# Kernel optimization log

Measured on AMD Instinct MI355X. Metric: run time of the kernel, lower is better.

Reference implementation:

```python
import jax, jax.numpy as jnp
import numpy as np

N, IN, HID, HEADS, OUT, E = 50000, 128, 64, 4, 128, 800000
NEG_SLOPE = 0.2


def _gat_conv(x, src, dst, W, a_src, a_dst, b, heads, ch, concat):
    # x: [N, F_in]; W: [F_in, heads*ch]; a_src/a_dst: [heads, ch]; b: [heads*ch] or [ch]
    n = x.shape[0]
    h = (x @ W).reshape(n, heads, ch)                       # [N,H,C]
    al_s = jnp.einsum('nhc,hc->nh', h, a_src)               # [N,H]
    al_d = jnp.einsum('nhc,hc->nh', h, a_dst)               # [N,H]
    e = jax.nn.leaky_relu(al_s[src] + al_d[dst], NEG_SLOPE)  # [E,H]
    # segment softmax over destination nodes (every node has a self-loop)
    m = jax.ops.segment_max(e, dst, num_segments=n)
    ex = jnp.exp(e - m[dst])
    denom = jax.ops.segment_sum(ex, dst, num_segments=n)
    alpha = ex / denom[dst]                                  # [E,H]
    msg = h[src] * alpha[:, :, None]                         # [E,H,C]
    out = jax.ops.segment_sum(msg, dst, num_segments=n)      # [N,H,C]
    out = out.reshape(n, heads * ch) if concat else out.mean(axis=1)
    return out + b


def setup_inputs() -> dict:
    key = jax.random.key(0)
    ks = jax.random.split(key, 10)
    s = 0.1
    return {
        'node_features': jax.random.normal(ks[0], (N, IN), jnp.float32),
        'edge_index': jax.random.randint(ks[1], (2, E), 0, N, jnp.int64),
        'W1': jax.random.normal(ks[2], (IN, HEADS * HID), jnp.float32) * s,
        'a1_src': jax.random.normal(ks[3], (HEADS, HID), jnp.float32) * s,
        'a1_dst': jax.random.normal(ks[4], (HEADS, HID), jnp.float32) * s,
        'b1': jnp.zeros((HEADS * HID,), jnp.float32),
        'W2': jax.random.normal(ks[5], (HEADS * HID, OUT), jnp.float32) * s,
        'a2_src': jax.random.normal(ks[6], (1, OUT), jnp.float32) * s,
        'a2_dst': jax.random.normal(ks[7], (1, OUT), jnp.float32) * s,
        'b2': jnp.zeros((OUT,), jnp.float32),
    }


def reference(node_features, edge_index, W1, a1_src, a1_dst, b1, W2, a2_src, a2_dst, b2):
    n = node_features.shape[0]
    loops = jnp.arange(n, dtype=edge_index.dtype)
    src = jnp.concatenate([edge_index[0], loops])  # PyG adds self-loops by default
    dst = jnp.concatenate([edge_index[1], loops])
    x = _gat_conv(node_features, src, dst, W1, a1_src, a1_dst, b1, HEADS, HID, True)
    x = jax.nn.relu(x)
    x = _gat_conv(x, src, dst, W2, a2_src, a2_dst, b2, 1, OUT, False)
    return x
```

## Files before the change

### kernel.cpp

```cpp
#include <hip/hip_runtime.h>
#include <math.h>

#define N_NODES 50000
#define F_IN    128
#define HIDC    64
#define HEADS   4
#define C1      (HEADS*HIDC)
#define F_OUT   128
#define NE      800000
#define NET     (NE + N_NODES)
#define NEG_SLOPE 0.2f

#define NPB   49
#define NBUCK 1021
#define BPAD  16
#define K4CAP 2048
#define SCHUNK 8192

typedef unsigned short ushort_t;
typedef signed char    schar_t;
typedef __attribute__((ext_vector_type(8))) short bf16x8;
typedef __attribute__((ext_vector_type(8))) unsigned short us8;
typedef __attribute__((ext_vector_type(4))) float f32x4;

__device__ __forceinline__ float b2f(ushort_t x) {
  return __uint_as_float(((unsigned int)x) << 16);
}
__device__ __forceinline__ ushort_t f2bf(float f) {
  unsigned int u = __float_as_uint(f);
  return (ushort_t)((u + 0x7fffu + ((u >> 16) & 1u)) >> 16);
}

__device__ __forceinline__ void fma8q(float wsc, uint2 vv, float* a) {
  int x = (int)vv.x, y = (int)vv.y;
  a[0] = fmaf(wsc, (float)(schar_t)(x),        a[0]);
  a[1] = fmaf(wsc, (float)(schar_t)(x >> 8),   a[1]);
  a[2] = fmaf(wsc, (float)(schar_t)(x >> 16),  a[2]);
  a[3] = fmaf(wsc, (float)(x >> 24),           a[3]);
  a[4] = fmaf(wsc, (float)(schar_t)(y),        a[4]);
  a[5] = fmaf(wsc, (float)(schar_t)(y >> 8),   a[5]);
  a[6] = fmaf(wsc, (float)(schar_t)(y >> 16),  a[6]);
  a[7] = fmaf(wsc, (float)(y >> 24),           a[7]);
}


__global__ __launch_bounds__(256) void bucket_count(const int* __restrict__ ei,
                                                    int* __restrict__ bcnt) {
  __shared__ int hist[NBUCK];
  for (int i = threadIdx.x; i < NBUCK; i += 256) hist[i] = 0;
  __syncthreads();
  int stride = gridDim.x * 256;
  for (int e = blockIdx.x * 256 + threadIdx.x; e < NET; e += stride) {
    int d = (e < NE) ? ei[NE + e] : (e - NE);
    atomicAdd(&hist[d / NPB], 1);
  }
  __syncthreads();
  for (int i = threadIdx.x; i < NBUCK; i += 256)
    if (hist[i]) atomicAdd(&bcnt[i * BPAD], hist[i]);
}

__global__ __launch_bounds__(1024) void scan_buckets(const int* __restrict__ bcnt,
                                                     int* __restrict__ boff) {
  __shared__ int sh[1024];
  int t = threadIdx.x;
  sh[t] = (t < NBUCK) ? bcnt[t * BPAD] : 0;
  __syncthreads();
#pragma unroll
  for (int off = 1; off < 1024; off <<= 1) {
    int u = (t >= off) ? sh[t - off] : 0;
    __syncthreads();
    sh[t] += u;
    __syncthreads();
  }
  if (t < NBUCK) boff[t + 1] = sh[t];
  if (t == 0) boff[0] = 0;
}

__global__ __launch_bounds__(1024) void bucket_scatter_blocked(const int* __restrict__ ei,
                                                               const int* __restrict__ boff,
                                                               int* __restrict__ bfill,
                                                               int2* __restrict__ pairs) {
  __shared__ int hist[NBUCK];
  __shared__ int gbase[NBUCK];
  __shared__ int fill[NBUCK];
  int c0 = blockIdx.x * SCHUNK;
  int cend = min(c0 + SCHUNK, NET);
  for (int i = threadIdx.x; i < NBUCK; i += 1024) { hist[i] = 0; fill[i] = 0; }
  __syncthreads();
  for (int e = c0 + threadIdx.x; e < cend; e += 1024) {
    int d = (e < NE) ? ei[NE + e] : (e - NE);
    atomicAdd(&hist[d / NPB], 1);
  }
  __syncthreads();
  for (int i = threadIdx.x; i < NBUCK; i += 1024)
    if (hist[i]) gbase[i] = boff[i] + atomicAdd(&bfill[i * BPAD], hist[i]);
  __syncthreads();
  for (int e = c0 + threadIdx.x; e < cend; e += 1024) {
    int s, d;
    if (e < NE) { s = ei[e]; d = ei[NE + e]; }
    else        { s = e - NE; d = s; }
    int b = d / NPB;
    int lpos = atomicAdd(&fill[b], 1);
    pairs[gbase[b] + lpos] = make_int2(s, d);
  }
}

__global__ __launch_bounds__(256) void build_csr(const int2* __restrict__ pairs,
                                                 const int* __restrict__ boff,
                                                 int* __restrict__ rowptr,
                                                 int* __restrict__ colsrc) {
  __shared__ int cnt[NPB];
  __shared__ int loc[NPB + 1];
  __shared__ int2 buf[K4CAP];
  int b = blockIdx.x, t = threadIdx.x;
  int p0 = boff[b], p1 = boff[b + 1];
  int m = p1 - p0;
  int n0 = b * NPB;
  int nn = min(NPB, N_NODES - n0);
  for (int i = t; i < NPB; i += 256) cnt[i] = 0;
  __syncthreads();
  bool inlds = (m <= K4CAP);
  for (int i = t; i < m; i += 256) {
    int2 p = pairs[p0 + i];
    if (inlds) buf[i] = p;
    atomicAdd(&cnt[p.y - n0], 1);
  }
  __syncthreads();
  if (t == 0) {
    int run = 0;
#pragma unroll 1
    for (int j = 0; j < nn; ++j) { loc[j] = run; run += cnt[j]; }
    loc[nn] = run;
  }
  __syncthreads();
  for (int j = t; j < nn; j += 256) rowptr[n0 + j] = p0 + loc[j];
  if (t == 0 && n0 + nn == N_NODES) rowptr[N_NODES] = NET;
  for (int i = t; i < NPB; i += 256) cnt[i] = 0;
  __syncthreads();
  for (int i = t; i < m; i += 256) {
    int2 p = inlds ? buf[i] : pairs[p0 + i];
    int j = p.y - n0;
    int pos = atomicAdd(&cnt[j], 1);
    colsrc[p0 + loc[j] + pos] = p.x;
  }
}


__global__ void transpose_both(const float* __restrict__ W1, ushort_t* __restrict__ W1t,
                               const float* __restrict__ W2, ushort_t* __restrict__ W2t) {
  int idx = blockIdx.x * blockDim.x + threadIdx.x;
  if (idx < F_IN * C1) {
    int k = idx / C1, n = idx - k * C1;
    W1t[(size_t)n * F_IN + k] = f2bf(W1[idx]);
  } else {
    int j = idx - F_IN * C1;
    if (j < C1 * F_OUT) {
      int k = j / F_OUT, n = j - k * F_OUT;
      W2t[(size_t)n * C1 + k] = f2bf(W2[j]);
    }
  }
}


#define BKS 64
#define LDT 72

__device__ __forceinline__ us8 stage8(const ushort_t* p) { return *(const us8*)p; }
__device__ __forceinline__ us8 stage8(const float* p) {
  float4 f0 = *(const float4*)p;
  float4 f1 = *(const float4*)(p + 4);
  us8 o;
  o[0] = f2bf(f0.x); o[1] = f2bf(f0.y); o[2] = f2bf(f0.z); o[3] = f2bf(f0.w);
  o[4] = f2bf(f1.x); o[5] = f2bf(f1.y); o[6] = f2bf(f1.z); o[7] = f2bf(f1.w);
  return o;
}

template<int K, int NCOL, int AL_MODE, int SCST, typename AT, typename CT>
__global__ __launch_bounds__(256) void gemm_mfma(const AT* __restrict__ A,
                                                 const ushort_t* __restrict__ Bt,
                                                 CT* __restrict__ C,
                                                 float* __restrict__ scales,
                                                 const float* __restrict__ a_s,
                                                 const float* __restrict__ a_d,
                                                 float* __restrict__ als,
                                                 float* __restrict__ ald) {
  __shared__ __align__(16) char smem[2 * 128 * LDT * 2];
  ushort_t (*Asl)[LDT] = (ushort_t(*)[LDT])smem;
  ushort_t (*Bsl)[LDT] = (ushort_t(*)[LDT])(smem + 128 * LDT * 2);

  const int tid = threadIdx.x;
  const int lane = tid & 63;
  const int wave = tid >> 6;
  const int wr = wave >> 1, wc = wave & 1;
  const int row0 = blockIdx.y * 128;
  const int col0 = blockIdx.x * 128;
  const int l15 = lane & 15, l4 = lane >> 4;

  f32x4 acc[4][4] = {};

  for (int k0 = 0; k0 < K; k0 += BKS) {
#pragma unroll
    for (int i = 0; i < 4; ++i) {
      int seg = tid + i * 256;
      int row = seg >> 3, kq = (seg & 7) * 8;
      int arow = row0 + row;
      us8 v = {0, 0, 0, 0, 0, 0, 0, 0};
      if (arow < N_NODES) v = stage8(&A[(size_t)arow * K + k0 + kq]);
      *(us8*)&Asl[row][kq] = v;
    }
#pragma unroll
    for (int i = 0; i < 4; ++i) {
      int seg = tid + i * 256;
      int row = seg >> 3, kq = (seg & 7) * 8;
      us8 v = *(const us8*)&Bt[(size_t)(col0 + row) * K + k0 + kq];
      *(us8*)&Bsl[row][kq] = v;
    }
    __syncthreads();
#pragma unroll
    for (int kk = 0; kk < BKS; kk += 32) {
      bf16x8 af[4], bfr[4];
#pragma unroll
      for (int mi = 0; mi < 4; ++mi)
        af[mi] = *(const bf16x8*)&Asl[wr * 64 + mi * 16 + l15][kk + l4 * 8];
#pragma unroll
      for (int ni = 0; ni < 4; ++ni)
        bfr[ni] = *(const bf16x8*)&Bsl[wc * 64 + ni * 16 + l15][kk + l4 * 8];
#pragma unroll
      for (int mi = 0; mi < 4; ++mi)
#pragma unroll
        for (int ni = 0; ni < 4; ++ni)
          acc[mi][ni] = __builtin_amdgcn_mfma_f32_16x16x32_bf16(af[mi], bfr[ni], acc[mi][ni], 0, 0, 0);
    }
    __syncthreads();
  }

  {
    const int albase = (AL_MODE == 1 ? col0 : 0) + wc * 64;
    float asv[4], adv[4];
#pragma unroll
    for (int ni = 0; ni < 4; ++ni) {
      asv[ni] = a_s[albase + ni * 16 + l15];
      adv[ni] = a_d[albase + ni * 16 + l15];
    }
#pragma unroll
    for (int mi = 0; mi < 4; ++mi) {
      float ps[4], pd[4];
#pragma unroll
      for (int r = 0; r < 4; ++r) {
        ps[r] = acc[mi][0][r] * asv[0] + acc[mi][1][r] * asv[1] +
                acc[mi][2][r] * asv[2] + acc[mi][3][r] * asv[3];
        pd[r] = acc[mi][0][r] * adv[0] + acc[mi][1][r] * adv[1] +
                acc[mi][2][r] * adv[2] + acc[mi][3][r] * adv[3];
      }
#pragma unroll
      for (int m = 1; m < 16; m <<= 1) {
#pragma unroll
        for (int r = 0; r < 4; ++r) {
          ps[r] += __shfl_xor(ps[r], m, 64);
          pd[r] += __shfl_xor(pd[r], m, 64);
        }
      }
      if (l15 == 0) {
#pragma unroll
        for (int r = 0; r < 4; ++r) {
          int row = row0 + wr * 64 + mi * 16 + l4 * 4 + r;
          if (row < N_NODES) {
            if (AL_MODE == 1) {
              int h = albase >> 6;
              als[row * 4 + h] = ps[r];
              ald[row * 4 + h] = pd[r];
            } else {
              atomicAdd(&als[row], ps[r]);
              atomicAdd(&ald[row], pd[r]);
            }
          }
        }
      }
    }
  }

  {
    ushort_t (*Ep)[136] = (ushort_t(*)[136])smem;
#pragma unroll
    for (int mi = 0; mi < 4; ++mi)
#pragma unroll
      for (int ni = 0; ni < 4; ++ni)
#pragma unroll
        for (int r = 0; r < 4; ++r)
          Ep[wr * 64 + mi * 16 + l4 * 4 + r][wc * 64 + ni * 16 + l15] = f2bf(acc[mi][ni][r]);
    __syncthreads();
    int row = tid >> 1, half = tid & 1;
    int grow = row0 + row;
    if (grow < N_NODES) {
      if constexpr (sizeof(CT) == 1) {
        float vals[64];
        float amax = 0.f;
#pragma unroll
        for (int i = 0; i < 8; ++i) {
          us8 v = *(const us8*)&Ep[row][half * 64 + i * 8];
#pragma unroll
          for (int j = 0; j < 8; ++j) {
            float f = b2f((ushort_t)v[j]);
            vals[i * 8 + j] = f;
            amax = fmaxf(amax, fabsf(f));
          }
        }
        float inv = amax > 0.f ? 127.f / amax : 0.f;
        scales[grow * SCST + (col0 >> 6) + half] = amax * (1.f / 127.f);
        schar_t ob[64];
#pragma unroll
        for (int i = 0; i < 64; ++i)
          ob[i] = (schar_t)(int)rintf(vals[i] * inv);
#pragma unroll
        for (int i = 0; i < 4; ++i)
          *(us8*)&C[(size_t)grow * NCOL + col0 + half * 64 + i * 16] =
              *(const us8*)&ob[i * 16];
      } else {
#pragma unroll
        for (int i = 0; i < 8; ++i)
          *(us8*)&C[(size_t)grow * NCOL + col0 + half * 64 + i * 8] =
              *(const us8*)&Ep[row][half * 64 + i * 8];
      }
    }
  }
}


__global__ __launch_bounds__(256) void agg1(const int* __restrict__ rowptr,
                                            const int* __restrict__ colsrc,
                                            const schar_t* __restrict__ Hq,
                                            const float* __restrict__ Sc,
                                            const float* __restrict__ als,
                                            const float* __restrict__ ald,
                                            const float* __restrict__ b1,
                                            ushort_t* __restrict__ X2b) {
  int wave = threadIdx.x >> 6, lane = threadIdx.x & 63;
  int n = blockIdx.x * 4 + wave;
  if (n >= N_NODES) return;
  int half = lane >> 5, li = lane & 31, h = li >> 3;
  float ad = ald[n * 4 + h];
  int beg = rowptr[n], end = rowptr[n + 1];
  float a[8] = {};
  float s = 0.f;
  int i = beg + half;
  for (; i + 6 < end; i += 8) {
    int s0 = colsrc[i], s1 = colsrc[i + 2], s2 = colsrc[i + 4], s3 = colsrc[i + 6];
    float sc0 = als[s0 * 4 + h] + ad;
    float sc1 = als[s1 * 4 + h] + ad;
    float sc2 = als[s2 * 4 + h] + ad;
    float sc3 = als[s3 * 4 + h] + ad;
    float q0 = Sc[s0 * 4 + h], q1 = Sc[s1 * 4 + h], q2 = Sc[s2 * 4 + h], q3 = Sc[s3 * 4 + h];
    uint2 v0 = *(const uint2*)&Hq[(size_t)s0 * C1 + li * 8];
    uint2 v1 = *(const uint2*)&Hq[(size_t)s1 * C1 + li * 8];
    uint2 v2 = *(const uint2*)&Hq[(size_t)s2 * C1 + li * 8];
    uint2 v3 = *(const uint2*)&Hq[(size_t)s3 * C1 + li * 8];
    sc0 = sc0 > 0.f ? sc0 : NEG_SLOPE * sc0;
    sc1 = sc1 > 0.f ? sc1 : NEG_SLOPE * sc1;
    sc2 = sc2 > 0.f ? sc2 : NEG_SLOPE * sc2;
    sc3 = sc3 > 0.f ? sc3 : NEG_SLOPE * sc3;
    float w0 = __expf(sc0), w1 = __expf(sc1), w2 = __expf(sc2), w3 = __expf(sc3);
    s += (w0 + w1) + (w2 + w3);
    fma8q(w0 * q0, v0, a); fma8q(w1 * q1, v1, a);
    fma8q(w2 * q2, v2, a); fma8q(w3 * q3, v3, a);
  }
  for (; i + 2 < end; i += 4) {
    int s0 = colsrc[i], s1 = colsrc[i + 2];
    float sc0 = als[s0 * 4 + h] + ad;
    float sc1 = als[s1 * 4 + h] + ad;
    float q0 = Sc[s0 * 4 + h], q1 = Sc[s1 * 4 + h];
    uint2 v0 = *(const uint2*)&Hq[(size_t)s0 * C1 + li * 8];
    uint2 v1 = *(const uint2*)&Hq[(size_t)s1 * C1 + li * 8];
    sc0 = sc0 > 0.f ? sc0 : NEG_SLOPE * sc0;
    sc1 = sc1 > 0.f ? sc1 : NEG_SLOPE * sc1;
    float w0 = __expf(sc0), w1 = __expf(sc1);
    s += w0 + w1;
    fma8q(w0 * q0, v0, a); fma8q(w1 * q1, v1, a);
  }
  for (; i < end; i += 2) {
    int s0 = colsrc[i];
    float sc0 = als[s0 * 4 + h] + ad;
    float q0 = Sc[s0 * 4 + h];
    uint2 v0 = *(const uint2*)&Hq[(size_t)s0 * C1 + li * 8];
    sc0 = sc0 > 0.f ? sc0 : NEG_SLOPE * sc0;
    float w0 = __expf(sc0);
    s += w0;
    fma8q(w0 * q0, v0, a);
  }
#pragma unroll
  for (int j = 0; j < 8; ++j) a[j] += __shfl_xor(a[j], 32, 64);
  s += __shfl_xor(s, 32, 64);
  if (lane < 32) {
    float si = 1.f / s;
    int c = li * 8;
    ushort_t o[8];
#pragma unroll
    for (int j = 0; j < 8; ++j)
      o[j] = f2bf(fmaxf(a[j] * si + b1[c + j], 0.f));
    *(us8*)&X2b[(size_t)n * C1 + c] = *(const us8*)o;
  }
}

__global__ __launch_bounds__(256) void agg2(const int* __restrict__ rowptr,
                                            const int* __restrict__ colsrc,
                                            const schar_t* __restrict__ Hq,
                                            const float* __restrict__ Sc,
                                            const float* __restrict__ als,
                                            const float* __restrict__ ald,
                                            const float* __restrict__ b2,
                                            float* __restrict__ out) {
  int wave = threadIdx.x >> 6, lane = threadIdx.x & 63;
  int n = blockIdx.x * 4 + wave;
  if (n >= N_NODES) return;
  int quarter = lane >> 4, li = lane & 15;
  int hb = li >> 3;
  float ad = ald[n];
  int beg = rowptr[n], end = rowptr[n + 1];
  float a[8] = {};
  float s = 0.f;
  int i = beg + quarter;
  for (; i + 4 < end; i += 8) {
    int s0 = colsrc[i], s1 = colsrc[i + 4];
    float sc0 = als[s0] + ad;
    float sc1 = als[s1] + ad;
    float q0 = Sc[s0 * 2 + hb], q1 = Sc[s1 * 2 + hb];
    uint2 v0 = *(const uint2*)&Hq[(size_t)s0 * F_OUT + li * 8];
    uint2 v1 = *(const uint2*)&Hq[(size_t)s1 * F_OUT + li * 8];
    sc0 = sc0 > 0.f ? sc0 : NEG_SLOPE * sc0;
    sc1 = sc1 > 0.f ? sc1 : NEG_SLOPE * sc1;
    float w0 = __expf(sc0), w1 = __expf(sc1);
    s += w0 + w1;
    fma8q(w0 * q0, v0, a); fma8q(w1 * q1, v1, a);
  }
  for (; i < end; i += 4) {
    int s0 = colsrc[i];
    float sc0 = als[s0] + ad;
    float q0 = Sc[s0 * 2 + hb];
    uint2 v0 = *(const uint2*)&Hq[(size_t)s0 * F_OUT + li * 8];
    sc0 = sc0 > 0.f ? sc0 : NEG_SLOPE * sc0;
    float w0 = __expf(sc0);
    s += w0;
    fma8q(w0 * q0, v0, a);
  }
#pragma unroll
  for (int j = 0; j < 8; ++j) a[j] += __shfl_xor(a[j], 16, 64);
#pragma unroll
  for (int j = 0; j < 8; ++j) a[j] += __shfl_xor(a[j], 32, 64);
  s += __shfl_xor(s, 16, 64);
  s += __shfl_xor(s, 32, 64);
  if (lane < 16) {
    float si = 1.f / s;
    int c = li * 8;
    float4 o0, o1;
    o0.x = a[0] * si + b2[c + 0]; o0.y = a[1] * si + b2[c + 1];
    o0.z = a[2] * si + b2[c + 2]; o0.w = a[3] * si + b2[c + 3];
    o1.x = a[4] * si + b2[c + 4]; o1.y = a[5] * si + b2[c + 5];
    o1.z = a[6] * si + b2[c + 6]; o1.w = a[7] * si + b2[c + 7];
    *(float4*)&out[(size_t)n * F_OUT + c] = o0;
    *(float4*)&out[(size_t)n * F_OUT + c + 4] = o1;
  }
}


extern "C" void kernel_launch(void* const* d_in, const int* in_sizes, int n_in,
                              void* d_out, int out_size, void* d_ws, size_t ws_size,
                              hipStream_t stream) {
  const float* X   = (const float*)d_in[0];
  const int*   EI  = (const int*)d_in[1];
  const float* W1  = (const float*)d_in[2];
  const float* a1s = (const float*)d_in[3];
  const float* a1d = (const float*)d_in[4];
  const float* b1  = (const float*)d_in[5];
  const float* W2  = (const float*)d_in[6];
  const float* a2s = (const float*)d_in[7];
  const float* a2d = (const float*)d_in[8];
  const float* b2  = (const float*)d_in[9];
  float* out = (float*)d_out;

  char* ws = (char*)d_ws;
  size_t off = 0;
  auto alloc = [&](size_t bytes) -> void* {
    void* p = ws + off;
    off += (bytes + 255) & ~(size_t)255;
    return p;
  };
  int* bcnt       = (int*)alloc((size_t)NBUCK * BPAD * 4);
  int* bfill      = (int*)alloc((size_t)NBUCK * BPAD * 4);
  float* ALS2     = (float*)alloc((size_t)N_NODES * 4);
  float* ALD2     = (float*)alloc((size_t)N_NODES * 4);
  size_t zero_span = off;
  int* boff       = (int*)alloc((size_t)(NBUCK + 1) * 4);
  int* rowptr     = (int*)alloc((size_t)(N_NODES + 1) * 4);
  int* colsrc     = (int*)alloc((size_t)NET * 4);
  int2* pairs     = (int2*)alloc((size_t)NET * 8);
  ushort_t* W1t   = (ushort_t*)alloc((size_t)C1 * F_IN * 2);
  ushort_t* W2t   = (ushort_t*)alloc((size_t)F_OUT * C1 * 2);
  schar_t* H1q    = (schar_t*)alloc((size_t)N_NODES * C1);
  float* SC1      = (float*)alloc((size_t)N_NODES * HEADS * 4);
  float* SC2      = (float*)alloc((size_t)N_NODES * 2 * 4);
  float* ALS1     = (float*)alloc((size_t)N_NODES * HEADS * 4);
  float* ALD1     = (float*)alloc((size_t)N_NODES * HEADS * 4);
  ushort_t* X2b   = (ushort_t*)alloc((size_t)N_NODES * C1 * 2);
  schar_t* H2q = H1q;

  hipMemsetAsync(ws, 0, zero_span, stream);

  bucket_count<<<128, 256, 0, stream>>>(EI, bcnt);
  scan_buckets<<<1, 1024, 0, stream>>>(bcnt, boff);
  bucket_scatter_blocked<<<(NET + SCHUNK - 1) / SCHUNK, 1024, 0, stream>>>(EI, boff, bfill, pairs);
  build_csr<<<NBUCK, 256, 0, stream>>>(pairs, boff, rowptr, colsrc);

  transpose_both<<<(F_IN * C1 + C1 * F_OUT + 255) / 256, 256, 0, stream>>>(W1, W1t, W2, W2t);

  {
    dim3 grid(C1 / 128, (N_NODES + 127) / 128);
    gemm_mfma<F_IN, C1, 1, 4, float, schar_t><<<grid, 256, 0, stream>>>(
        X, W1t, H1q, SC1, a1s, a1d, ALS1, ALD1);
  }
  agg1<<<(N_NODES + 3) / 4, 256, 0, stream>>>(rowptr, colsrc, H1q, SC1, ALS1, ALD1, b1, X2b);

  {
    dim3 grid(F_OUT / 128, (N_NODES + 127) / 128);
    gemm_mfma<C1, F_OUT, 2, 2, ushort_t, schar_t><<<grid, 256, 0, stream>>>(
        X2b, W2t, H2q, SC2, a2s, a2d, ALS2, ALD2);
  }
  agg2<<<(N_NODES + 3) / 4, 256, 0, stream>>>(rowptr, colsrc, H2q, SC2, ALS2, ALD2, b2, out);
}
```

Baseline: 170.8 us.

## Merge setup kernels and co-schedule GEMM1 with edge bucket scatter

Fuses the bucket count with the weight transpose in one launch, and runs the first-layer GEMM and the edge bucket scatter as disjoint block ranges of a single kernel. The aim is to cut two kernel launches and let the memory-bound scatter overlap the compute-bound GEMM. The scatter blocks now use 256 threads instead of 1024 and share the GEMM's shared-memory buffer, so each scatter block runs longer and the combined kernel's occupancy is tied to the GEMM's resources.

```diff
diff --git a/kernel.cpp b/kernel.cpp
--- a/kernel.cpp
+++ b/kernel.cpp
@@ -16,12 +16,21 @@
 #define BPAD  16
 #define K4CAP 2048
 #define SCHUNK 8192
+#define GEMM1_BX (C1 / 128)
+#define GEMM1_BY ((N_NODES + 127) / 128)
+#define GEMM1_BLOCKS (GEMM1_BX * GEMM1_BY)
+#define SCAT_BLOCKS ((NET + SCHUNK - 1) / SCHUNK)
+#define CNT_BLOCKS 128
+#define TRN_ELEMS (F_IN * C1 + C1 * F_OUT)
+#define TRN_BLOCKS (TRN_ELEMS / 256)
 
 typedef unsigned short ushort_t;
 typedef signed char    schar_t;
 typedef __attribute__((ext_vector_type(8))) short bf16x8;
 typedef __attribute__((ext_vector_type(8))) unsigned short us8;
 typedef __attribute__((ext_vector_type(4))) float f32x4;
+
+#define SMEMSZ (2 * 128 * 72 * 2)
 
 __device__ __forceinline__ float b2f(ushort_t x) {
   return __uint_as_float(((unsigned int)x) << 16);
@@ -44,19 +53,36 @@
 }
 
 
-__global__ __launch_bounds__(256) void bucket_count(const int* __restrict__ ei,
-                                                    int* __restrict__ bcnt) {
+__global__ __launch_bounds__(256) void setup_fused(const int* __restrict__ ei,
+                                                   int* __restrict__ bcnt,
+                                                   const float* __restrict__ W1,
+                                                   ushort_t* __restrict__ W1t,
+                                                   const float* __restrict__ W2,
+                                                   ushort_t* __restrict__ W2t) {
   __shared__ int hist[NBUCK];
-  for (int i = threadIdx.x; i < NBUCK; i += 256) hist[i] = 0;
-  __syncthreads();
-  int stride = gridDim.x * 256;
-  for (int e = blockIdx.x * 256 + threadIdx.x; e < NET; e += stride) {
-    int d = (e < NE) ? ei[NE + e] : (e - NE);
-    atomicAdd(&hist[d / NPB], 1);
-  }
-  __syncthreads();
-  for (int i = threadIdx.x; i < NBUCK; i += 256)
-    if (hist[i]) atomicAdd(&bcnt[i * BPAD], hist[i]);
+  int bid = blockIdx.x;
+  if (bid < CNT_BLOCKS) {
+    for (int i = threadIdx.x; i < NBUCK; i += 256) hist[i] = 0;
+    __syncthreads();
+    int stride = CNT_BLOCKS * 256;
+    for (int e = bid * 256 + threadIdx.x; e < NET; e += stride) {
+      int d = (e < NE) ? ei[NE + e] : (e - NE);
+      atomicAdd(&hist[d / NPB], 1);
+    }
+    __syncthreads();
+    for (int i = threadIdx.x; i < NBUCK; i += 256)
+      if (hist[i]) atomicAdd(&bcnt[i * BPAD], hist[i]);
+  } else {
+    int idx = (bid - CNT_BLOCKS) * 256 + threadIdx.x;
+    if (idx < F_IN * C1) {
+      int k = idx / C1, n = idx - k * C1;
+      W1t[(size_t)n * F_IN + k] = f2bf(W1[idx]);
+    } else if (idx < TRN_ELEMS) {
+      int j = idx - F_IN * C1;
+      int k = j / F_OUT, n = j - k * F_OUT;
+      W2t[(size_t)n * C1 + k] = f2bf(W2[j]);
+    }
+  }
 }
 
 __global__ __launch_bounds__(1024) void scan_buckets(const int* __restrict__ bcnt,
@@ -76,32 +102,218 @@
   if (t == 0) boff[0] = 0;
 }
 
-__global__ __launch_bounds__(1024) void bucket_scatter_blocked(const int* __restrict__ ei,
-                                                               const int* __restrict__ boff,
-                                                               int* __restrict__ bfill,
-                                                               int2* __restrict__ pairs) {
-  __shared__ int hist[NBUCK];
-  __shared__ int gbase[NBUCK];
-  __shared__ int fill[NBUCK];
-  int c0 = blockIdx.x * SCHUNK;
-  int cend = min(c0 + SCHUNK, NET);
-  for (int i = threadIdx.x; i < NBUCK; i += 1024) { hist[i] = 0; fill[i] = 0; }
-  __syncthreads();
-  for (int e = c0 + threadIdx.x; e < cend; e += 1024) {
-    int d = (e < NE) ? ei[NE + e] : (e - NE);
-    atomicAdd(&hist[d / NPB], 1);
-  }
-  __syncthreads();
-  for (int i = threadIdx.x; i < NBUCK; i += 1024)
-    if (hist[i]) gbase[i] = boff[i] + atomicAdd(&bfill[i * BPAD], hist[i]);
-  __syncthreads();
-  for (int e = c0 + threadIdx.x; e < cend; e += 1024) {
-    int s, d;
-    if (e < NE) { s = ei[e]; d = ei[NE + e]; }
-    else        { s = e - NE; d = s; }
-    int b = d / NPB;
-    int lpos = atomicAdd(&fill[b], 1);
-    pairs[gbase[b] + lpos] = make_int2(s, d);
+
+#define BKS 64
+#define LDT 72
+
+__device__ __forceinline__ us8 stage8(const ushort_t* p) { return *(const us8*)p; }
+__device__ __forceinline__ us8 stage8(const float* p) {
+  float4 f0 = *(const float4*)p;
+  float4 f1 = *(const float4*)(p + 4);
+  us8 o;
+  o[0] = f2bf(f0.x); o[1] = f2bf(f0.y); o[2] = f2bf(f0.z); o[3] = f2bf(f0.w);
+  o[4] = f2bf(f1.x); o[5] = f2bf(f1.y); o[6] = f2bf(f1.z); o[7] = f2bf(f1.w);
+  return o;
+}
+
+template<int K, int NCOL, int AL_MODE, int SCST, typename AT, typename CT>
+__device__ void gemm_body(char* smem, int bx, int by,
+                          const AT* __restrict__ A, const ushort_t* __restrict__ Bt,
+                          CT* __restrict__ C, float* __restrict__ scales,
+                          const float* __restrict__ a_s, const float* __restrict__ a_d,
+                          float* __restrict__ als, float* __restrict__ ald) {
+  ushort_t (*Asl)[LDT] = (ushort_t(*)[LDT])smem;
+  ushort_t (*Bsl)[LDT] = (ushort_t(*)[LDT])(smem + 128 * LDT * 2);
+
+  const int tid = threadIdx.x;
+  const int lane = tid & 63;
+  const int wave = tid >> 6;
+  const int wr = wave >> 1, wc = wave & 1;
+  const int row0 = by * 128;
+  const int col0 = bx * 128;
+  const int l15 = lane & 15, l4 = lane >> 4;
+
+  f32x4 acc[4][4] = {};
+
+  for (int k0 = 0; k0 < K; k0 += BKS) {
+#pragma unroll
+    for (int i = 0; i < 4; ++i) {
+      int seg = tid + i * 256;
+      int row = seg >> 3, kq = (seg & 7) * 8;
+      int arow = row0 + row;
+      us8 v = {0, 0, 0, 0, 0, 0, 0, 0};
+      if (arow < N_NODES) v = stage8(&A[(size_t)arow * K + k0 + kq]);
+      *(us8*)&Asl[row][kq] = v;
+    }
+#pragma unroll
+    for (int i = 0; i < 4; ++i) {
+      int seg = tid + i * 256;
+      int row = seg >> 3, kq = (seg & 7) * 8;
+      us8 v = *(const us8*)&Bt[(size_t)(col0 + row) * K + k0 + kq];
+      *(us8*)&Bsl[row][kq] = v;
+    }
+    __syncthreads();
+#pragma unroll
+    for (int kk = 0; kk < BKS; kk += 32) {
+      bf16x8 af[4], bfr[4];
+#pragma unroll
+      for (int mi = 0; mi < 4; ++mi)
+        af[mi] = *(const bf16x8*)&Asl[wr * 64 + mi * 16 + l15][kk + l4 * 8];
+#pragma unroll
+      for (int ni = 0; ni < 4; ++ni)
+        bfr[ni] = *(const bf16x8*)&Bsl[wc * 64 + ni * 16 + l15][kk + l4 * 8];
+#pragma unroll
+      for (int mi = 0; mi < 4; ++mi)
+#pragma unroll
+        for (int ni = 0; ni < 4; ++ni)
+          acc[mi][ni] = __builtin_amdgcn_mfma_f32_16x16x32_bf16(af[mi], bfr[ni], acc[mi][ni], 0, 0, 0);
+    }
+    __syncthreads();
+  }
+
+  {
+    const int albase = (AL_MODE == 1 ? col0 : 0) + wc * 64;
+    float asv[4], adv[4];
+#pragma unroll
+    for (int ni = 0; ni < 4; ++ni) {
+      asv[ni] = a_s[albase + ni * 16 + l15];
+      adv[ni] = a_d[albase + ni * 16 + l15];
+    }
+#pragma unroll
+    for (int mi = 0; mi < 4; ++mi) {
+      float ps[4], pd[4];
+#pragma unroll
+      for (int r = 0; r < 4; ++r) {
+        ps[r] = acc[mi][0][r] * asv[0] + acc[mi][1][r] * asv[1] +
+                acc[mi][2][r] * asv[2] + acc[mi][3][r] * asv[3];
+        pd[r] = acc[mi][0][r] * adv[0] + acc[mi][1][r] * adv[1] +
+                acc[mi][2][r] * adv[2] + acc[mi][3][r] * adv[3];
+      }
+#pragma unroll
+      for (int m = 1; m < 16; m <<= 1) {
+#pragma unroll
+        for (int r = 0; r < 4; ++r) {
+          ps[r] += __shfl_xor(ps[r], m, 64);
+          pd[r] += __shfl_xor(pd[r], m, 64);
+        }
+      }
+      if (l15 == 0) {
+#pragma unroll
+        for (int r = 0; r < 4; ++r) {
+          int row = row0 + wr * 64 + mi * 16 + l4 * 4 + r;
+          if (row < N_NODES) {
+            if (AL_MODE == 1) {
+              int h = albase >> 6;
+              als[row * 4 + h] = ps[r];
+              ald[row * 4 + h] = pd[r];
+            } else {
+              atomicAdd(&als[row], ps[r]);
+              atomicAdd(&ald[row], pd[r]);
+            }
+          }
+        }
+      }
+    }
+  }
+
+  {
+    ushort_t (*Ep)[136] = (ushort_t(*)[136])smem;
+#pragma unroll
+    for (int mi = 0; mi < 4; ++mi)
+#pragma unroll
+      for (int ni = 0; ni < 4; ++ni)
+#pragma unroll
+        for (int r = 0; r < 4; ++r)
+          Ep[wr * 64 + mi * 16 + l4 * 4 + r][wc * 64 + ni * 16 + l15] = f2bf(acc[mi][ni][r]);
+    __syncthreads();
+    int row = tid >> 1, half = tid & 1;
+    int grow = row0 + row;
+    if (grow < N_NODES) {
+      if constexpr (sizeof(CT) == 1) {
+        float vals[64];
+        float amax = 0.f;
+#pragma unroll
+        for (int i = 0; i < 8; ++i) {
+          us8 v = *(const us8*)&Ep[row][half * 64 + i * 8];
+#pragma unroll
+          for (int j = 0; j < 8; ++j) {
+            float f = b2f((ushort_t)v[j]);
+            vals[i * 8 + j] = f;
+            amax = fmaxf(amax, fabsf(f));
+          }
+        }
+        float inv = amax > 0.f ? 127.f / amax : 0.f;
+        scales[grow * SCST + (col0 >> 6) + half] = amax * (1.f / 127.f);
+        schar_t ob[64];
+#pragma unroll
+        for (int i = 0; i < 64; ++i)
+          ob[i] = (schar_t)(int)rintf(vals[i] * inv);
+#pragma unroll
+        for (int i = 0; i < 4; ++i)
+          *(us8*)&C[(size_t)grow * NCOL + col0 + half * 64 + i * 16] =
+              *(const us8*)&ob[i * 16];
+      } else {
+#pragma unroll
+        for (int i = 0; i < 8; ++i)
+          *(us8*)&C[(size_t)grow * NCOL + col0 + half * 64 + i * 8] =
+              *(const us8*)&Ep[row][half * 64 + i * 8];
+      }
+    }
+  }
+}
+
+template<int K, int NCOL, int AL_MODE, int SCST, typename AT, typename CT>
+__global__ __launch_bounds__(256) void gemm_mfma(const AT* __restrict__ A,
+                                                 const ushort_t* __restrict__ Bt,
+                                                 CT* __restrict__ C,
+                                                 float* __restrict__ scales,
+                                                 const float* __restrict__ a_s,
+                                                 const float* __restrict__ a_d,
+                                                 float* __restrict__ als,
+                                                 float* __restrict__ ald) {
+  __shared__ __align__(16) char smem[SMEMSZ];
+  gemm_body<K, NCOL, AL_MODE, SCST, AT, CT>(smem, blockIdx.x, blockIdx.y,
+                                            A, Bt, C, scales, a_s, a_d, als, ald);
+}
+
+
+__global__ __launch_bounds__(256) void gemm1_plus_scatter(
+    const float* __restrict__ X, const ushort_t* __restrict__ W1t,
+    schar_t* __restrict__ H1q, float* __restrict__ SC1,
+    const float* __restrict__ a1s, const float* __restrict__ a1d,
+    float* __restrict__ ALS1, float* __restrict__ ALD1,
+    const int* __restrict__ ei, const int* __restrict__ boff,
+    int* __restrict__ bfill, int2* __restrict__ pairs) {
+  __shared__ __align__(16) char smem[SMEMSZ];
+  int bid = blockIdx.x;
+  if (bid < GEMM1_BLOCKS) {
+    gemm_body<F_IN, C1, 1, 4, float, schar_t>(smem, bid % GEMM1_BX, bid / GEMM1_BX,
+                                              X, W1t, H1q, SC1, a1s, a1d, ALS1, ALD1);
+  } else {
+    int* hist  = (int*)smem;
+    int* gbase = hist + NBUCK;
+    int* fill  = gbase + NBUCK;
+    int chunk = bid - GEMM1_BLOCKS;
+    int c0 = chunk * SCHUNK;
+    int cend = min(c0 + SCHUNK, NET);
+    for (int i = threadIdx.x; i < NBUCK; i += 256) { hist[i] = 0; fill[i] = 0; }
+    __syncthreads();
+    for (int e = c0 + threadIdx.x; e < cend; e += 256) {
+      int d = (e < NE) ? ei[NE + e] : (e - NE);
+      atomicAdd(&hist[d / NPB], 1);
+    }
+    __syncthreads();
+    for (int i = threadIdx.x; i < NBUCK; i += 256)
+      if (hist[i]) gbase[i] = boff[i] + atomicAdd(&bfill[i * BPAD], hist[i]);
+    __syncthreads();
+    for (int e = c0 + threadIdx.x; e < cend; e += 256) {
+      int s, d;
+      if (e < NE) { s = ei[e]; d = ei[NE + e]; }
+      else        { s = e - NE; d = s; }
+      int b = d / NPB;
+      int lpos = atomicAdd(&fill[b], 1);
+      pairs[gbase[b] + lpos] = make_int2(s, d);
+    }
   }
 }
 
@@ -142,186 +354,6 @@
     int j = p.y - n0;
     int pos = atomicAdd(&cnt[j], 1);
     colsrc[p0 + loc[j] + pos] = p.x;
-  }
-}
-
-
-__global__ void transpose_both(const float* __restrict__ W1, ushort_t* __restrict__ W1t,
-                               const float* __restrict__ W2, ushort_t* __restrict__ W2t) {
-  int idx = blockIdx.x * blockDim.x + threadIdx.x;
-  if (idx < F_IN * C1) {
-    int k = idx / C1, n = idx - k * C1;
-    W1t[(size_t)n * F_IN + k] = f2bf(W1[idx]);
-  } else {
-    int j = idx - F_IN * C1;
-    if (j < C1 * F_OUT) {
-      int k = j / F_OUT, n = j - k * F_OUT;
-      W2t[(size_t)n * C1 + k] = f2bf(W2[j]);
-    }
-  }
-}
-
-
-#define BKS 64
-#define LDT 72
-
-__device__ __forceinline__ us8 stage8(const ushort_t* p) { return *(const us8*)p; }
-__device__ __forceinline__ us8 stage8(const float* p) {
-  float4 f0 = *(const float4*)p;
-  float4 f1 = *(const float4*)(p + 4);
-  us8 o;
-  o[0] = f2bf(f0.x); o[1] = f2bf(f0.y); o[2] = f2bf(f0.z); o[3] = f2bf(f0.w);
-  o[4] = f2bf(f1.x); o[5] = f2bf(f1.y); o[6] = f2bf(f1.z); o[7] = f2bf(f1.w);
-  return o;
-}
-
-template<int K, int NCOL, int AL_MODE, int SCST, typename AT, typename CT>
-__global__ __launch_bounds__(256) void gemm_mfma(const AT* __restrict__ A,
-                                                 const ushort_t* __restrict__ Bt,
-                                                 CT* __restrict__ C,
-                                                 float* __restrict__ scales,
-                                                 const float* __restrict__ a_s,
-                                                 const float* __restrict__ a_d,
-                                                 float* __restrict__ als,
-                                                 float* __restrict__ ald) {
-  __shared__ __align__(16) char smem[2 * 128 * LDT * 2];
-  ushort_t (*Asl)[LDT] = (ushort_t(*)[LDT])smem;
-  ushort_t (*Bsl)[LDT] = (ushort_t(*)[LDT])(smem + 128 * LDT * 2);
-
-  const int tid = threadIdx.x;
-  const int lane = tid & 63;
-  const int wave = tid >> 6;
-  const int wr = wave >> 1, wc = wave & 1;
-  const int row0 = blockIdx.y * 128;
-  const int col0 = blockIdx.x * 128;
-  const int l15 = lane & 15, l4 = lane >> 4;
-
-  f32x4 acc[4][4] = {};
-
-  for (int k0 = 0; k0 < K; k0 += BKS) {
-#pragma unroll
-    for (int i = 0; i < 4; ++i) {
-      int seg = tid + i * 256;
-      int row = seg >> 3, kq = (seg & 7) * 8;
-      int arow = row0 + row;
-      us8 v = {0, 0, 0, 0, 0, 0, 0, 0};
-      if (arow < N_NODES) v = stage8(&A[(size_t)arow * K + k0 + kq]);
-      *(us8*)&Asl[row][kq] = v;
-    }
-#pragma unroll
-    for (int i = 0; i < 4; ++i) {
-      int seg = tid + i * 256;
-      int row = seg >> 3, kq = (seg & 7) * 8;
-      us8 v = *(const us8*)&Bt[(size_t)(col0 + row) * K + k0 + kq];
-      *(us8*)&Bsl[row][kq] = v;
-    }
-    __syncthreads();
-#pragma unroll
-    for (int kk = 0; kk < BKS; kk += 32) {
-      bf16x8 af[4], bfr[4];
-#pragma unroll
-      for (int mi = 0; mi < 4; ++mi)
-        af[mi] = *(const bf16x8*)&Asl[wr * 64 + mi * 16 + l15][kk + l4 * 8];
-#pragma unroll
-      for (int ni = 0; ni < 4; ++ni)
-        bfr[ni] = *(const bf16x8*)&Bsl[wc * 64 + ni * 16 + l15][kk + l4 * 8];
-#pragma unroll
-      for (int mi = 0; mi < 4; ++mi)
-#pragma unroll
-        for (int ni = 0; ni < 4; ++ni)
-          acc[mi][ni] = __builtin_amdgcn_mfma_f32_16x16x32_bf16(af[mi], bfr[ni], acc[mi][ni], 0, 0, 0);
-    }
-    __syncthreads();
-  }
-
-  {
-    const int albase = (AL_MODE == 1 ? col0 : 0) + wc * 64;
-    float asv[4], adv[4];
-#pragma unroll
-    for (int ni = 0; ni < 4; ++ni) {
-      asv[ni] = a_s[albase + ni * 16 + l15];
-      adv[ni] = a_d[albase + ni * 16 + l15];
-    }
-#pragma unroll
-    for (int mi = 0; mi < 4; ++mi) {
-      float ps[4], pd[4];
-#pragma unroll
-      for (int r = 0; r < 4; ++r) {
-        ps[r] = acc[mi][0][r] * asv[0] + acc[mi][1][r] * asv[1] +
-                acc[mi][2][r] * asv[2] + acc[mi][3][r] * asv[3];
-        pd[r] = acc[mi][0][r] * adv[0] + acc[mi][1][r] * adv[1] +
-                acc[mi][2][r] * adv[2] + acc[mi][3][r] * adv[3];
-      }
-#pragma unroll
-      for (int m = 1; m < 16; m <<= 1) {
-#pragma unroll
-        for (int r = 0; r < 4; ++r) {
-          ps[r] += __shfl_xor(ps[r], m, 64);
-          pd[r] += __shfl_xor(pd[r], m, 64);
-        }
-      }
-      if (l15 == 0) {
-#pragma unroll
-        for (int r = 0; r < 4; ++r) {
-          int row = row0 + wr * 64 + mi * 16 + l4 * 4 + r;
-          if (row < N_NODES) {
-            if (AL_MODE == 1) {
-              int h = albase >> 6;
-              als[row * 4 + h] = ps[r];
-              ald[row * 4 + h] = pd[r];
-            } else {
-              atomicAdd(&als[row], ps[r]);
-              atomicAdd(&ald[row], pd[r]);
-            }
-          }
-        }
-      }
-    }
-  }
-
-  {
-    ushort_t (*Ep)[136] = (ushort_t(*)[136])smem;
-#pragma unroll
-    for (int mi = 0; mi < 4; ++mi)
-#pragma unroll
-      for (int ni = 0; ni < 4; ++ni)
-#pragma unroll
-        for (int r = 0; r < 4; ++r)
-          Ep[wr * 64 + mi * 16 + l4 * 4 + r][wc * 64 + ni * 16 + l15] = f2bf(acc[mi][ni][r]);
-    __syncthreads();
-    int row = tid >> 1, half = tid & 1;
-    int grow = row0 + row;
-    if (grow < N_NODES) {
-      if constexpr (sizeof(CT) == 1) {
-        float vals[64];
-        float amax = 0.f;
-#pragma unroll
-        for (int i = 0; i < 8; ++i) {
-          us8 v = *(const us8*)&Ep[row][half * 64 + i * 8];
-#pragma unroll
-          for (int j = 0; j < 8; ++j) {
-            float f = b2f((ushort_t)v[j]);
-            vals[i * 8 + j] = f;
-            amax = fmaxf(amax, fabsf(f));
-          }
-        }
-        float inv = amax > 0.f ? 127.f / amax : 0.f;
-        scales[grow * SCST + (col0 >> 6) + half] = amax * (1.f / 127.f);
-        schar_t ob[64];
-#pragma unroll
-        for (int i = 0; i < 64; ++i)
-          ob[i] = (schar_t)(int)rintf(vals[i] * inv);
-#pragma unroll
-        for (int i = 0; i < 4; ++i)
-          *(us8*)&C[(size_t)grow * NCOL + col0 + half * 64 + i * 16] =
-              *(const us8*)&ob[i * 16];
-      } else {
-#pragma unroll
-        for (int i = 0; i < 8; ++i)
-          *(us8*)&C[(size_t)grow * NCOL + col0 + half * 64 + i * 8] =
-              *(const us8*)&Ep[row][half * 64 + i * 8];
-      }
-    }
   }
 }
 
@@ -504,20 +536,12 @@
 
   hipMemsetAsync(ws, 0, zero_span, stream);
 
-  bucket_count<<<128, 256, 0, stream>>>(EI, bcnt);
+  setup_fused<<<CNT_BLOCKS + TRN_BLOCKS, 256, 0, stream>>>(EI, bcnt, W1, W1t, W2, W2t);
   scan_buckets<<<1, 1024, 0, stream>>>(bcnt, boff);
-  bucket_scatter_blocked<<<(NET + SCHUNK - 1) / SCHUNK, 1024, 0, stream>>>(EI, boff, bfill, pairs);
+  gemm1_plus_scatter<<<GEMM1_BLOCKS + SCAT_BLOCKS, 256, 0, stream>>>(
+      X, W1t, H1q, SC1, a1s, a1d, ALS1, ALD1, EI, boff, bfill, pairs);
   build_csr<<<NBUCK, 256, 0, stream>>>(pairs, boff, rowptr, colsrc);
-
-  transpose_both<<<(F_IN * C1 + C1 * F_OUT + 255) / 256, 256, 0, stream>>>(W1, W1t, W2, W2t);
-
-  {
-    dim3 grid(C1 / 128, (N_NODES + 127) / 128);
-    gemm_mfma<F_IN, C1, 1, 4, float, schar_t><<<grid, 256, 0, stream>>>(
-        X, W1t, H1q, SC1, a1s, a1d, ALS1, ALD1);
-  }
   agg1<<<(N_NODES + 3) / 4, 256, 0, stream>>>(rowptr, colsrc, H1q, SC1, ALS1, ALD1, b1, X2b);
-
   {
     dim3 grid(F_OUT / 128, (N_NODES + 127) / 128);
     gemm_mfma<C1, F_OUT, 2, 2, ushort_t, schar_t><<<grid, 256, 0, stream>>>(
```

After: 168.8 us. No clear change (-1.1%).

## Fuse bucket count, weight transpose and X bf16 cast into one setup kernel

Applied to the files above, without the earlier changes.

Merges the edge bucket histogram, the weight transpose/convert and a new pre-cast of X to bf16 into a single launch, split across blocks by block index. The first GEMM now reads pre-converted bf16 X instead of converting fp32 inside its staging loop, and build_csr is moved after the first GEMM. The aim is to cut launch count, shrink the GEMM's load and convert work and reorder independent stages. The price is an extra bf16 copy of X written and read back through memory.

```diff
diff --git a/kernel.cpp b/kernel.cpp
--- a/kernel.cpp
+++ b/kernel.cpp
@@ -16,6 +16,10 @@
 #define BPAD  16
 #define K4CAP 2048
 #define SCHUNK 8192
+#define CNT_BLOCKS 128
+#define TRN_ELEMS (F_IN * C1 + C1 * F_OUT)
+#define TRN_BLOCKS (TRN_ELEMS / 256)
+#define CASTX_BLOCKS (N_NODES * F_IN / 8 / 256)
 
 typedef unsigned short ushort_t;
 typedef signed char    schar_t;
@@ -43,20 +47,52 @@
   a[7] = fmaf(wsc, (float)(y >> 24),           a[7]);
 }
 
-
-__global__ __launch_bounds__(256) void bucket_count(const int* __restrict__ ei,
-                                                    int* __restrict__ bcnt) {
+__device__ __forceinline__ us8 pack8(const float* p) {
+  float4 f0 = *(const float4*)p;
+  float4 f1 = *(const float4*)(p + 4);
+  us8 o;
+  o[0] = f2bf(f0.x); o[1] = f2bf(f0.y); o[2] = f2bf(f0.z); o[3] = f2bf(f0.w);
+  o[4] = f2bf(f1.x); o[5] = f2bf(f1.y); o[6] = f2bf(f1.z); o[7] = f2bf(f1.w);
+  return o;
+}
+
+
+__global__ __launch_bounds__(256) void setup_fused(const int* __restrict__ ei,
+                                                   int* __restrict__ bcnt,
+                                                   const float* __restrict__ W1,
+                                                   ushort_t* __restrict__ W1t,
+                                                   const float* __restrict__ W2,
+                                                   ushort_t* __restrict__ W2t,
+                                                   const float* __restrict__ X,
+                                                   ushort_t* __restrict__ Xb) {
   __shared__ int hist[NBUCK];
-  for (int i = threadIdx.x; i < NBUCK; i += 256) hist[i] = 0;
-  __syncthreads();
-  int stride = gridDim.x * 256;
-  for (int e = blockIdx.x * 256 + threadIdx.x; e < NET; e += stride) {
-    int d = (e < NE) ? ei[NE + e] : (e - NE);
-    atomicAdd(&hist[d / NPB], 1);
-  }
-  __syncthreads();
-  for (int i = threadIdx.x; i < NBUCK; i += 256)
-    if (hist[i]) atomicAdd(&bcnt[i * BPAD], hist[i]);
+  int bid = blockIdx.x;
+  if (bid < CNT_BLOCKS) {
+    for (int i = threadIdx.x; i < NBUCK; i += 256) hist[i] = 0;
+    __syncthreads();
+    int stride = CNT_BLOCKS * 256;
+    for (int e = bid * 256 + threadIdx.x; e < NET; e += stride) {
+      int d = (e < NE) ? ei[NE + e] : (e - NE);
+      atomicAdd(&hist[d / NPB], 1);
+    }
+    __syncthreads();
+    for (int i = threadIdx.x; i < NBUCK; i += 256)
+      if (hist[i]) atomicAdd(&bcnt[i * BPAD], hist[i]);
+  } else if (bid < CNT_BLOCKS + TRN_BLOCKS) {
+    int idx = (bid - CNT_BLOCKS) * 256 + threadIdx.x;
+    if (idx < F_IN * C1) {
+      int k = idx / C1, n = idx - k * C1;
+      W1t[(size_t)n * F_IN + k] = f2bf(W1[idx]);
+    } else {
+      int j = idx - F_IN * C1;
+      int k = j / F_OUT, n = j - k * F_OUT;
+      W2t[(size_t)n * C1 + k] = f2bf(W2[j]);
+    }
+  } else {
+    int seg = (bid - CNT_BLOCKS - TRN_BLOCKS) * 256 + threadIdx.x;
+    if (seg * 8 < N_NODES * F_IN)
+      *(us8*)&Xb[(size_t)seg * 8] = pack8(&X[(size_t)seg * 8]);
+  }
 }
 
 __global__ __launch_bounds__(1024) void scan_buckets(const int* __restrict__ bcnt,
@@ -146,37 +182,11 @@
 }
 
 
-__global__ void transpose_both(const float* __restrict__ W1, ushort_t* __restrict__ W1t,
-                               const float* __restrict__ W2, ushort_t* __restrict__ W2t) {
-  int idx = blockIdx.x * blockDim.x + threadIdx.x;
-  if (idx < F_IN * C1) {
-    int k = idx / C1, n = idx - k * C1;
-    W1t[(size_t)n * F_IN + k] = f2bf(W1[idx]);
-  } else {
-    int j = idx - F_IN * C1;
-    if (j < C1 * F_OUT) {
-      int k = j / F_OUT, n = j - k * F_OUT;
-      W2t[(size_t)n * C1 + k] = f2bf(W2[j]);
-    }
-  }
-}
-
-
 #define BKS 64
 #define LDT 72
 
-__device__ __forceinline__ us8 stage8(const ushort_t* p) { return *(const us8*)p; }
-__device__ __forceinline__ us8 stage8(const float* p) {
-  float4 f0 = *(const float4*)p;
-  float4 f1 = *(const float4*)(p + 4);
-  us8 o;
-  o[0] = f2bf(f0.x); o[1] = f2bf(f0.y); o[2] = f2bf(f0.z); o[3] = f2bf(f0.w);
-  o[4] = f2bf(f1.x); o[5] = f2bf(f1.y); o[6] = f2bf(f1.z); o[7] = f2bf(f1.w);
-  return o;
-}
-
-template<int K, int NCOL, int AL_MODE, int SCST, typename AT, typename CT>
-__global__ __launch_bounds__(256) void gemm_mfma(const AT* __restrict__ A,
+template<int K, int NCOL, int AL_MODE, int SCST, typename CT>
+__global__ __launch_bounds__(256) void gemm_mfma(const ushort_t* __restrict__ A,
                                                  const ushort_t* __restrict__ Bt,
                                                  CT* __restrict__ C,
                                                  float* __restrict__ scales,
@@ -205,7 +215,7 @@
       int row = seg >> 3, kq = (seg & 7) * 8;
       int arow = row0 + row;
       us8 v = {0, 0, 0, 0, 0, 0, 0, 0};
-      if (arow < N_NODES) v = stage8(&A[(size_t)arow * K + k0 + kq]);
+      if (arow < N_NODES) v = *(const us8*)&A[(size_t)arow * K + k0 + kq];
       *(us8*)&Asl[row][kq] = v;
     }
 #pragma unroll
@@ -494,6 +504,7 @@
   int2* pairs     = (int2*)alloc((size_t)NET * 8);
   ushort_t* W1t   = (ushort_t*)alloc((size_t)C1 * F_IN * 2);
   ushort_t* W2t   = (ushort_t*)alloc((size_t)F_OUT * C1 * 2);
+  ushort_t* Xb    = (ushort_t*)alloc((size_t)N_NODES * F_IN * 2);
   schar_t* H1q    = (schar_t*)alloc((size_t)N_NODES * C1);
   float* SC1      = (float*)alloc((size_t)N_NODES * HEADS * 4);
   float* SC2      = (float*)alloc((size_t)N_NODES * 2 * 4);
@@ -504,23 +515,20 @@
 
   hipMemsetAsync(ws, 0, zero_span, stream);
 
-  bucket_count<<<128, 256, 0, stream>>>(EI, bcnt);
+  setup_fused<<<CNT_BLOCKS + TRN_BLOCKS + CASTX_BLOCKS, 256, 0, stream>>>(
+      EI, bcnt, W1, W1t, W2, W2t, X, Xb);
   scan_buckets<<<1, 1024, 0, stream>>>(bcnt, boff);
   bucket_scatter_blocked<<<(NET + SCHUNK - 1) / SCHUNK, 1024, 0, stream>>>(EI, boff, bfill, pairs);
-  build_csr<<<NBUCK, 256, 0, stream>>>(pairs, boff, rowptr, colsrc);
-
-  transpose_both<<<(F_IN * C1 + C1 * F_OUT + 255) / 256, 256, 0, stream>>>(W1, W1t, W2, W2t);
-
   {
     dim3 grid(C1 / 128, (N_NODES + 127) / 128);
-    gemm_mfma<F_IN, C1, 1, 4, float, schar_t><<<grid, 256, 0, stream>>>(
-        X, W1t, H1q, SC1, a1s, a1d, ALS1, ALD1);
-  }
+    gemm_mfma<F_IN, C1, 1, 4, schar_t><<<grid, 256, 0, stream>>>(
+        Xb, W1t, H1q, SC1, a1s, a1d, ALS1, ALD1);
+  }
+  build_csr<<<NBUCK, 256, 0, stream>>>(pairs, boff, rowptr, colsrc);
   agg1<<<(N_NODES + 3) / 4, 256, 0, stream>>>(rowptr, colsrc, H1q, SC1, ALS1, ALD1, b1, X2b);
-
   {
     dim3 grid(F_OUT / 128, (N_NODES + 127) / 128);
-    gemm_mfma<C1, F_OUT, 2, 2, ushort_t, schar_t><<<grid, 256, 0, stream>>>(
+    gemm_mfma<C1, F_OUT, 2, 2, schar_t><<<grid, 256, 0, stream>>>(
         X2b, W2t, H2q, SC2, a2s, a2d, ALS2, ALD2);
   }
   agg2<<<(N_NODES + 3) / 4, 256, 0, stream>>>(rowptr, colsrc, H2q, SC2, ALS2, ALD2, b2, out);
```

Result: no change. 168.8 us (-1.2%).
